# Kernel tuning notes

Hardware: AMD Instinct MI355X
Metric: run time of the kernel (lower is better)

Reference implementation:

```python
import jax, jax.numpy as jnp
import numpy as np

B, T_TGT, T_SRC, H, V = 4, 256, 512, 1024, 32100


def setup_inputs() -> dict:
    key = jax.random.key(0)
    ks = jax.random.split(key, 7)
    return {
        "decoder_hidden_states": jax.random.normal(ks[0], (B, T_TGT, H), dtype=jnp.float32),
        "cross_attention_weights": jax.random.uniform(ks[1], (B, T_TGT, T_SRC), dtype=jnp.float32),
        "encoder_hidden_states": jax.random.normal(ks[2], (B, T_SRC, H), dtype=jnp.float32),
        "vocab_logits": jax.random.normal(ks[3], (B, T_TGT, V), dtype=jnp.float32),
        "W_gen": jax.random.normal(ks[4], (2 * H, 1), dtype=jnp.float32) * (1.0 / np.sqrt(2 * H)),
        "b_gen": jnp.zeros((1,), dtype=jnp.float32),
        "source_ids": jax.random.randint(ks[5], (B, T_SRC), 0, V, dtype=jnp.int64).astype(jnp.int32),
        "vocab_size": V,
    }


def reference(decoder_hidden_states, cross_attention_weights, encoder_hidden_states,
              vocab_logits, W_gen, b_gen, source_ids, vocab_size):
    # context vector: (B, T_tgt, H) = attn (B,T_tgt,T_src) @ enc (B,T_src,H)
    context = jnp.einsum('bts,bsh->bth', cross_attention_weights, encoder_hidden_states)
    gen_input = jnp.concatenate([context, decoder_hidden_states], axis=-1)  # (B,T_tgt,2H)
    p_gen = jax.nn.sigmoid(gen_input @ W_gen + b_gen)  # (B,T_tgt,1)

    vocab_dist = jax.nn.softmax(vocab_logits, axis=-1)  # (B,T_tgt,V)

    # scatter-add attention mass onto vocab ids; duplicates accumulate
    def scatter_one(ids, attn):  # ids (T_src,), attn (T_tgt,T_src)
        return jnp.zeros((attn.shape[0], vocab_size), attn.dtype).at[:, ids].add(attn)

    copy_dist = jax.vmap(scatter_one)(source_ids, cross_attention_weights)  # (B,T_tgt,V)

    final_dist = p_gen * vocab_dist + (1.0 - p_gen) * copy_dist + 1e-12
    return jnp.log(final_dist)
```

## Files before the change

### kernel.cpp

```cpp
#include <hip/hip_runtime.h>
#include <math.h>

#define NB 4
#define TT 256
#define TS 512
#define HH 1024
#define VV 32100
#define V4 8025
#define NCHUNK 4
#define C4 2007
#define CF (C4 * 4)
#define NT 512

__global__ __launch_bounds__(256) void precompute_dots(
    const float* __restrict__ dec, const float* __restrict__ enc,
    const float* __restrict__ Wg, const float* __restrict__ bg,
    float* __restrict__ e, float* __restrict__ g2)
{
    int row  = blockIdx.x * 4 + (threadIdx.x >> 6);
    int lane = threadIdx.x & 63;

    const float4* s4;
    const float4* w4;
    float bias = 0.0f;
    float* dst;

    if (row < NB * TS) {
        s4  = (const float4*)(enc + (size_t)row * HH);
        w4  = (const float4*)Wg;
        dst = e + row;
    } else {
        int rr = row - NB * TS;
        if (rr >= NB * TT) return;
        s4   = (const float4*)(dec + (size_t)rr * HH);
        w4   = (const float4*)(Wg + HH);
        bias = bg[0];
        dst  = g2 + rr;
    }

    float acc = 0.0f;
#pragma unroll
    for (int i = lane; i < HH / 4; i += 64) {
        float4 a = s4[i];
        float4 w = w4[i];
        acc += a.x * w.x + a.y * w.y + a.z * w.z + a.w * w.w;
    }
#pragma unroll
    for (int off = 32; off >= 1; off >>= 1)
        acc += __shfl_xor(acc, off);
    if (lane == 0) *dst = acc + bias;
}

__global__ __launch_bounds__(NT, 8) void pointer_gen_kernel(
    const float* __restrict__ attn, const int* __restrict__ ids,
    const float* __restrict__ logits, const float* __restrict__ e,
    const float* __restrict__ g2, float* __restrict__ out)
{
    __shared__ float chunk[CF];
    __shared__ float redd[8];
    __shared__ float redm[8];
    __shared__ float reds[8];
    __shared__ float bcast[3];

    const int tid  = threadIdx.x;
    const int bt   = blockIdx.x;
    const int b    = bt >> 8;
    const int wid  = tid >> 6;
    const int lane = tid & 63;

    const float av  = attn[(size_t)bt * TS + tid];
    const int   idv = ids[b * TS + tid];

    float part = av * e[b * TS + tid];
#pragma unroll
    for (int off = 32; off >= 1; off >>= 1)
        part += __shfl_xor(part, off);
    if (lane == 0) redd[wid] = part;

    const float4* lp = (const float4*)(logits + (size_t)bt * VV);
    float mi = -3.4e38f, si = 0.0f;
    for (int i = tid; i < V4; i += NT) {
        float4 v  = lp[i];
        float  m4 = fmaxf(fmaxf(v.x, v.y), fmaxf(v.z, v.w));
        if (m4 > mi) { si *= __expf(mi - m4); mi = m4; }
        si += __expf(v.x - mi) + __expf(v.y - mi) +
              __expf(v.z - mi) + __expf(v.w - mi);
    }
#pragma unroll
    for (int off = 32; off >= 1; off >>= 1) {
        float om = __shfl_xor(mi, off);
        float os = __shfl_xor(si, off);
        float nm = fmaxf(mi, om);
        si = si * __expf(mi - nm) + os * __expf(om - nm);
        mi = nm;
    }
    if (lane == 0) { redm[wid] = mi; reds[wid] = si; }
    __syncthreads();

    if (wid == 0) {
        float d = (lane < 8) ? redd[lane] : 0.0f;
#pragma unroll
        for (int off = 4; off >= 1; off >>= 1)
            d += __shfl_xor(d, off);
        float m = (lane < 8) ? redm[lane] : -3.4e38f;
        float s = (lane < 8) ? reds[lane] : 0.0f;
#pragma unroll
        for (int off = 4; off >= 1; off >>= 1) {
            float om = __shfl_xor(m, off);
            float os = __shfl_xor(s, off);
            float nm = fmaxf(m, om);
            s = s * __expf(m - nm) + os * __expf(om - nm);
            m = nm;
        }
        if (lane == 0) {
            float pg = 1.0f / (1.0f + __expf(-(d + g2[bt])));
            bcast[0] = m;
            bcast[1] = s;
            bcast[2] = pg;
        }
    }
    __syncthreads();

    const float m  = bcast[0];
    const float pg = bcast[2];
    const float pz = pg / bcast[1];
    const float q  = 1.0f - pg;

    float4* op = (float4*)(out + (size_t)bt * VV);
    const float4 z4 = make_float4(0.f, 0.f, 0.f, 0.f);

    for (int c = 0; c < NCHUNK; ++c) {
        const int lo    = c * CF;
        const int base4 = c * C4;
        const int top4  = (base4 + C4 < V4) ? (base4 + C4) : V4;

        for (int i = tid; i < C4; i += NT)
            ((float4*)chunk)[i] = z4;
        __syncthreads();

        if (idv >= lo && idv < lo + CF)
            atomicAdd(&chunk[idv - lo], av);
        __syncthreads();

        for (int i = base4 + tid; i < top4; i += NT) {
            float4 v = lp[i];
            float4 cc = ((const float4*)chunk)[i - base4];
            float4 o;
            o.x = __logf(fmaf(pz, __expf(v.x - m), fmaf(q, cc.x, 1e-12f)));
            o.y = __logf(fmaf(pz, __expf(v.y - m), fmaf(q, cc.y, 1e-12f)));
            o.z = __logf(fmaf(pz, __expf(v.z - m), fmaf(q, cc.z, 1e-12f)));
            o.w = __logf(fmaf(pz, __expf(v.w - m), fmaf(q, cc.w, 1e-12f)));
            op[i] = o;
        }
        __syncthreads();
    }
}

extern "C" void kernel_launch(void* const* d_in, const int* in_sizes, int n_in,
                              void* d_out, int out_size, void* d_ws, size_t ws_size,
                              hipStream_t stream) {
    const float* dec    = (const float*)d_in[0];
    const float* attn   = (const float*)d_in[1];
    const float* enc    = (const float*)d_in[2];
    const float* logits = (const float*)d_in[3];
    const float* Wg     = (const float*)d_in[4];
    const float* bg     = (const float*)d_in[5];
    const int*   ids    = (const int*)d_in[6];
    float* out = (float*)d_out;

    float* e  = (float*)d_ws;
    float* g2 = e + NB * TS;

    precompute_dots<<<(NB * TS + NB * TT) / 4, 256, 0, stream>>>(
        dec, enc, Wg, bg, e, g2);

    pointer_gen_kernel<<<NB * TT, NT, 0, stream>>>(
        attn, ids, logits, e, g2, out);
}
```

Baseline: 68.40 us.

## Cache logits row in registers to avoid second global read pass

Each thread now loads its whole share of the logits row (16 float4s) into registers once, finds the max and then the sum-exp in two register passes, and reuses the same registers for the output pass. Before, the row was read from global memory twice, once for the online softmax and once for the output. The launch bound is relaxed from 8 to 4 waves per SIMD to make room for the 64 extra registers, which lowers occupancy and removes the memory-level parallelism of the streaming loops.

New measurement: 60.34 us. 11.8% less time.

```diff
diff --git a/kernel.cpp b/kernel.cpp
--- a/kernel.cpp
+++ b/kernel.cpp
@@ -11,6 +11,7 @@
 #define C4 2007
 #define CF (C4 * 4)
 #define NT 512
+#define KREG 16
 
 __global__ __launch_bounds__(256) void precompute_dots(
     const float* __restrict__ dec, const float* __restrict__ enc,
@@ -51,7 +52,7 @@
     if (lane == 0) *dst = acc + bias;
 }
 
-__global__ __launch_bounds__(NT, 8) void pointer_gen_kernel(
+__global__ __launch_bounds__(NT, 4) void pointer_gen_kernel(
     const float* __restrict__ attn, const int* __restrict__ ids,
     const float* __restrict__ logits, const float* __restrict__ e,
     const float* __restrict__ g2, float* __restrict__ out)
@@ -70,31 +71,52 @@
 
     const float av  = attn[(size_t)bt * TS + tid];
     const int   idv = ids[b * TS + tid];
-
     float part = av * e[b * TS + tid];
+
+    const float4* lp = (const float4*)(logits + (size_t)bt * VV);
+    float4 v[KREG];
+#pragma unroll
+    for (int k = 0; k < KREG; ++k) {
+        int f  = tid + NT * k;
+        int fc = (f < V4) ? f : (V4 - 1);
+        v[k] = lp[fc];
+    }
+
 #pragma unroll
     for (int off = 32; off >= 1; off >>= 1)
         part += __shfl_xor(part, off);
     if (lane == 0) redd[wid] = part;
 
-    const float4* lp = (const float4*)(logits + (size_t)bt * VV);
-    float mi = -3.4e38f, si = 0.0f;
-    for (int i = tid; i < V4; i += NT) {
-        float4 v  = lp[i];
-        float  m4 = fmaxf(fmaxf(v.x, v.y), fmaxf(v.z, v.w));
-        if (m4 > mi) { si *= __expf(mi - m4); mi = m4; }
-        si += __expf(v.x - mi) + __expf(v.y - mi) +
-              __expf(v.z - mi) + __expf(v.w - mi);
+    float mt = -3.4e38f;
+#pragma unroll
+    for (int k = 0; k < KREG; ++k) {
+        float4 w = v[k];
+        mt = fmaxf(mt, fmaxf(fmaxf(w.x, w.y), fmaxf(w.z, w.w)));
+    }
+    float st = 0.0f;
+#pragma unroll
+    for (int k = 0; k < KREG - 1; ++k) {
+        float4 w = v[k];
+        st += __expf(w.x - mt) + __expf(w.y - mt) +
+              __expf(w.z - mt) + __expf(w.w - mt);
+    }
+    {
+        int f = tid + NT * (KREG - 1);
+        if (f < V4) {
+            float4 w = v[KREG - 1];
+            st += __expf(w.x - mt) + __expf(w.y - mt) +
+                  __expf(w.z - mt) + __expf(w.w - mt);
+        }
     }
 #pragma unroll
     for (int off = 32; off >= 1; off >>= 1) {
-        float om = __shfl_xor(mi, off);
-        float os = __shfl_xor(si, off);
-        float nm = fmaxf(mi, om);
-        si = si * __expf(mi - nm) + os * __expf(om - nm);
-        mi = nm;
-    }
-    if (lane == 0) { redm[wid] = mi; reds[wid] = si; }
+        float om = __shfl_xor(mt, off);
+        float os = __shfl_xor(st, off);
+        float nm = fmaxf(mt, om);
+        st = st * __expf(mt - nm) + os * __expf(om - nm);
+        mt = nm;
+    }
+    if (lane == 0) { redm[wid] = mt; reds[wid] = st; }
     __syncthreads();
 
     if (wid == 0) {
@@ -129,28 +151,37 @@
     float4* op = (float4*)(out + (size_t)bt * VV);
     const float4 z4 = make_float4(0.f, 0.f, 0.f, 0.f);
 
+#pragma unroll
     for (int c = 0; c < NCHUNK; ++c) {
-        const int lo    = c * CF;
-        const int base4 = c * C4;
-        const int top4  = (base4 + C4 < V4) ? (base4 + C4) : V4;
-
-        for (int i = tid; i < C4; i += NT)
-            ((float4*)chunk)[i] = z4;
+        const int flo = C4 * c;
+        const int fhi = flo + C4;
+
+#pragma unroll
+        for (int i = 0; i < 4; ++i) {
+            int j = tid + NT * i;
+            if (j < C4) ((float4*)chunk)[j] = z4;
+        }
         __syncthreads();
 
-        if (idv >= lo && idv < lo + CF)
-            atomicAdd(&chunk[idv - lo], av);
+        if (idv >= 4 * flo && idv < 4 * fhi)
+            atomicAdd(&chunk[idv - 4 * flo], av);
         __syncthreads();
 
-        for (int i = base4 + tid; i < top4; i += NT) {
-            float4 v = lp[i];
-            float4 cc = ((const float4*)chunk)[i - base4];
-            float4 o;
-            o.x = __logf(fmaf(pz, __expf(v.x - m), fmaf(q, cc.x, 1e-12f)));
-            o.y = __logf(fmaf(pz, __expf(v.y - m), fmaf(q, cc.y, 1e-12f)));
-            o.z = __logf(fmaf(pz, __expf(v.z - m), fmaf(q, cc.z, 1e-12f)));
-            o.w = __logf(fmaf(pz, __expf(v.w - m), fmaf(q, cc.w, 1e-12f)));
-            op[i] = o;
+#pragma unroll
+        for (int k = 0; k < KREG; ++k) {
+            if (NT * k + NT - 1 >= flo && NT * k < fhi) {
+                int f = tid + NT * k;
+                if (f >= flo && f < fhi && f < V4) {
+                    float4 cc = ((const float4*)chunk)[f - flo];
+                    float4 w  = v[k];
+                    float4 o;
+                    o.x = __logf(fmaf(pz, __expf(w.x - m), fmaf(q, cc.x, 1e-12f)));
+                    o.y = __logf(fmaf(pz, __expf(w.y - m), fmaf(q, cc.y, 1e-12f)));
+                    o.z = __logf(fmaf(pz, __expf(w.z - m), fmaf(q, cc.z, 1e-12f)));
+                    o.w = __logf(fmaf(pz, __expf(w.w - m), fmaf(q, cc.w, 1e-12f)));
+                    op[f] = o;
+                }
+            }
         }
         __syncthreads();
     }
```

## Split pointer-gen kernel into stats pass and per-chunk output kernel

Applied to the files above, without the earlier changes.

The fused per-row kernel is split in two. A stats kernel computes the softmax max/sum and p_gen per row, using two interleaved online-softmax accumulators and a fully unrolled load loop. An output kernel then runs one block per (row, vocab chunk), so the four chunks run in parallel instead of serially with syncs inside one block. This adds a kernel launch and a small global stats buffer, and every block in the output pass re-reads attention and ids.

Result: slower. 72.06 us (+5.3%).

```diff
diff --git a/kernel.cpp b/kernel.cpp
--- a/kernel.cpp
+++ b/kernel.cpp
@@ -10,7 +10,6 @@
 #define NCHUNK 4
 #define C4 2007
 #define CF (C4 * 4)
-#define NT 512
 
 __global__ __launch_bounds__(256) void precompute_dots(
     const float* __restrict__ dec, const float* __restrict__ enc,
@@ -51,108 +50,135 @@
     if (lane == 0) *dst = acc + bias;
 }
 
-__global__ __launch_bounds__(NT, 8) void pointer_gen_kernel(
+#define ACC0(a)                                                     \
+    { float ma = fmaxf(fmaxf(a.x, a.y), fmaxf(a.z, a.w));           \
+      if (ma > m0) { s0 *= __expf(m0 - ma); m0 = ma; }              \
+      s0 += __expf(a.x - m0) + __expf(a.y - m0) +                   \
+            __expf(a.z - m0) + __expf(a.w - m0); }
+#define ACC1(a)                                                     \
+    { float ma = fmaxf(fmaxf(a.x, a.y), fmaxf(a.z, a.w));           \
+      if (ma > m1) { s1 *= __expf(m1 - ma); m1 = ma; }              \
+      s1 += __expf(a.x - m1) + __expf(a.y - m1) +                   \
+            __expf(a.z - m1) + __expf(a.w - m1); }
+
+__global__ __launch_bounds__(256) void stats_kernel(
+    const float* __restrict__ attn, const float* __restrict__ logits,
+    const float* __restrict__ e, const float* __restrict__ g2,
+    float4* __restrict__ stats)
+{
+    __shared__ float redm[4], reds[4], redd[4];
+
+    const int bt   = blockIdx.x;
+    const int b    = bt >> 8;
+    const int tid  = threadIdx.x;
+    const int wid  = tid >> 6;
+    const int lane = tid & 63;
+
+    float part = attn[(size_t)bt * TS + tid]       * e[b * TS + tid]
+               + attn[(size_t)bt * TS + 256 + tid] * e[b * TS + 256 + tid];
+
+    const float4* lp = (const float4*)(logits + (size_t)bt * VV);
+    float m0 = -3.4e38f, s0 = 0.0f, m1 = -3.4e38f, s1 = 0.0f;
+
+#pragma unroll
+    for (int k = 0; k < 30; k += 2) {
+        float4 a = lp[tid + 256 * k];
+        float4 c = lp[tid + 256 * (k + 1)];
+        ACC0(a)
+        ACC1(c)
+    }
+    {
+        float4 a = lp[tid + 256 * 30];
+        ACC0(a)
+    }
+    {
+        int f = tid + 256 * 31;
+        if (f < V4) {
+            float4 c = lp[f];
+            ACC1(c)
+        }
+    }
+    {
+        float nm = fmaxf(m0, m1);
+        s0 = s0 * __expf(m0 - nm) + s1 * __expf(m1 - nm);
+        m0 = nm;
+    }
+#pragma unroll
+    for (int off = 32; off >= 1; off >>= 1) {
+        float om = __shfl_xor(m0, off);
+        float os = __shfl_xor(s0, off);
+        float nm = fmaxf(m0, om);
+        s0 = s0 * __expf(m0 - nm) + os * __expf(om - nm);
+        m0 = nm;
+        part += __shfl_xor(part, off);
+    }
+    if (lane == 0) { redm[wid] = m0; reds[wid] = s0; redd[wid] = part; }
+    __syncthreads();
+
+    if (tid == 0) {
+        float m = redm[0], s = reds[0];
+#pragma unroll
+        for (int w = 1; w < 4; ++w) {
+            float nm = fmaxf(m, redm[w]);
+            s = s * __expf(m - nm) + reds[w] * __expf(redm[w] - nm);
+            m = nm;
+        }
+        float d  = redd[0] + redd[1] + redd[2] + redd[3];
+        float pg = 1.0f / (1.0f + __expf(-(d + g2[bt])));
+        stats[bt] = make_float4(m, s, pg, 0.0f);
+    }
+}
+
+__global__ __launch_bounds__(512) void out_kernel(
     const float* __restrict__ attn, const int* __restrict__ ids,
-    const float* __restrict__ logits, const float* __restrict__ e,
-    const float* __restrict__ g2, float* __restrict__ out)
+    const float* __restrict__ logits, const float4* __restrict__ stats,
+    float* __restrict__ out)
 {
     __shared__ float chunk[CF];
-    __shared__ float redd[8];
-    __shared__ float redm[8];
-    __shared__ float reds[8];
-    __shared__ float bcast[3];
-
-    const int tid  = threadIdx.x;
-    const int bt   = blockIdx.x;
-    const int b    = bt >> 8;
-    const int wid  = tid >> 6;
-    const int lane = tid & 63;
+
+    const int blk = blockIdx.x;
+    const int bt  = blk >> 2;
+    const int c   = blk & 3;
+    const int b   = bt >> 8;
+    const int tid = threadIdx.x;
+
+    const float4 z4 = make_float4(0.f, 0.f, 0.f, 0.f);
+#pragma unroll
+    for (int i = 0; i < 4; ++i) {
+        int j = tid + 512 * i;
+        if (j < C4) ((float4*)chunk)[j] = z4;
+    }
 
     const float av  = attn[(size_t)bt * TS + tid];
     const int   idv = ids[b * TS + tid];
-
-    float part = av * e[b * TS + tid];
-#pragma unroll
-    for (int off = 32; off >= 1; off >>= 1)
-        part += __shfl_xor(part, off);
-    if (lane == 0) redd[wid] = part;
+    const float4 st = stats[bt];
+    __syncthreads();
+
+    const int lo = c * CF;
+    if (idv >= lo && idv < lo + CF)
+        atomicAdd(&chunk[idv - lo], av);
+    __syncthreads();
+
+    const float m  = st.x;
+    const float pg = st.z;
+    const float pz = pg / st.y;
+    const float q  = 1.0f - pg;
 
     const float4* lp = (const float4*)(logits + (size_t)bt * VV);
-    float mi = -3.4e38f, si = 0.0f;
-    for (int i = tid; i < V4; i += NT) {
-        float4 v  = lp[i];
-        float  m4 = fmaxf(fmaxf(v.x, v.y), fmaxf(v.z, v.w));
-        if (m4 > mi) { si *= __expf(mi - m4); mi = m4; }
-        si += __expf(v.x - mi) + __expf(v.y - mi) +
-              __expf(v.z - mi) + __expf(v.w - mi);
-    }
-#pragma unroll
-    for (int off = 32; off >= 1; off >>= 1) {
-        float om = __shfl_xor(mi, off);
-        float os = __shfl_xor(si, off);
-        float nm = fmaxf(mi, om);
-        si = si * __expf(mi - nm) + os * __expf(om - nm);
-        mi = nm;
-    }
-    if (lane == 0) { redm[wid] = mi; reds[wid] = si; }
-    __syncthreads();
-
-    if (wid == 0) {
-        float d = (lane < 8) ? redd[lane] : 0.0f;
-#pragma unroll
-        for (int off = 4; off >= 1; off >>= 1)
-            d += __shfl_xor(d, off);
-        float m = (lane < 8) ? redm[lane] : -3.4e38f;
-        float s = (lane < 8) ? reds[lane] : 0.0f;
-#pragma unroll
-        for (int off = 4; off >= 1; off >>= 1) {
-            float om = __shfl_xor(m, off);
-            float os = __shfl_xor(s, off);
-            float nm = fmaxf(m, om);
-            s = s * __expf(m - nm) + os * __expf(om - nm);
-            m = nm;
-        }
-        if (lane == 0) {
-            float pg = 1.0f / (1.0f + __expf(-(d + g2[bt])));
-            bcast[0] = m;
-            bcast[1] = s;
-            bcast[2] = pg;
-        }
-    }
-    __syncthreads();
-
-    const float m  = bcast[0];
-    const float pg = bcast[2];
-    const float pz = pg / bcast[1];
-    const float q  = 1.0f - pg;
-
-    float4* op = (float4*)(out + (size_t)bt * VV);
-    const float4 z4 = make_float4(0.f, 0.f, 0.f, 0.f);
-
-    for (int c = 0; c < NCHUNK; ++c) {
-        const int lo    = c * CF;
-        const int base4 = c * C4;
-        const int top4  = (base4 + C4 < V4) ? (base4 + C4) : V4;
-
-        for (int i = tid; i < C4; i += NT)
-            ((float4*)chunk)[i] = z4;
-        __syncthreads();
-
-        if (idv >= lo && idv < lo + CF)
-            atomicAdd(&chunk[idv - lo], av);
-        __syncthreads();
-
-        for (int i = base4 + tid; i < top4; i += NT) {
-            float4 v = lp[i];
-            float4 cc = ((const float4*)chunk)[i - base4];
-            float4 o;
-            o.x = __logf(fmaf(pz, __expf(v.x - m), fmaf(q, cc.x, 1e-12f)));
-            o.y = __logf(fmaf(pz, __expf(v.y - m), fmaf(q, cc.y, 1e-12f)));
-            o.z = __logf(fmaf(pz, __expf(v.z - m), fmaf(q, cc.z, 1e-12f)));
-            o.w = __logf(fmaf(pz, __expf(v.w - m), fmaf(q, cc.w, 1e-12f)));
-            op[i] = o;
-        }
-        __syncthreads();
+    float4*       op = (float4*)(out + (size_t)bt * VV);
+    const int flo = c * C4;
+    const int fhi = (flo + C4 < V4) ? (flo + C4) : V4;
+
+#pragma unroll
+    for (int f = flo + tid; f < fhi; f += 512) {
+        float4 v  = lp[f];
+        float4 cc = ((const float4*)chunk)[f - flo];
+        float4 o;
+        o.x = __logf(fmaf(pz, __expf(v.x - m), fmaf(q, cc.x, 1e-12f)));
+        o.y = __logf(fmaf(pz, __expf(v.y - m), fmaf(q, cc.y, 1e-12f)));
+        o.z = __logf(fmaf(pz, __expf(v.z - m), fmaf(q, cc.z, 1e-12f)));
+        o.w = __logf(fmaf(pz, __expf(v.w - m), fmaf(q, cc.w, 1e-12f)));
+        op[f] = o;
     }
 }
 
@@ -168,12 +194,15 @@
     const int*   ids    = (const int*)d_in[6];
     float* out = (float*)d_out;
 
-    float* e  = (float*)d_ws;
-    float* g2 = e + NB * TS;
+    float*  e     = (float*)d_ws;
+    float*  g2    = e + NB * TS;
+    float4* stats = (float4*)(g2 + NB * TT);
 
     precompute_dots<<<(NB * TS + NB * TT) / 4, 256, 0, stream>>>(
         dec, enc, Wg, bg, e, g2);
 
-    pointer_gen_kernel<<<NB * TT, NT, 0, stream>>>(
-        attn, ids, logits, e, g2, out);
-}
+    stats_kernel<<<NB * TT, 256, 0, stream>>>(attn, logits, e, g2, stats);
+
+    out_kernel<<<NB * TT * NCHUNK, 512, 0, stream>>>(
+        attn, ids, logits, stats, out);
+}
```
